# Kernel optimization log

Hardware: AMD Instinct MI355X
Metric: run time of the kernel (lower is better)

## Reference

```python
import jax, jax.numpy as jnp
import numpy as np
from jax.scipy.special import i0

# Module config (init_kwargs). sector_width only affects CUDA tiling, not math.
OSF = 2
KERNEL_WIDTH = 3
IMG_DIM = 320
B, M = 8, 200000


def setup_inputs() -> dict:
    key = jax.random.key(0)
    k1, k2, k3, k4 = jax.random.split(key, 4)
    x_re = jax.random.normal(k1, (B, IMG_DIM, IMG_DIM), jnp.float32)
    x_im = jax.random.normal(k2, (B, IMG_DIM, IMG_DIM), jnp.float32)
    # normalized k-space trajectory in [-0.5, 0.5) (gpuNUFFT convention)
    traj = jax.random.uniform(k3, (B, 2, M), jnp.float32, -0.5, 0.5)
    # density compensation weights, strictly positive
    dcf = jax.random.uniform(k4, (B, M), jnp.float32, 0.01, 1.0)
    return {"x_re": x_re, "x_im": x_im, "traj": traj, "dcf": dcf}


def _kb(d, W, beta):
    # Kaiser-Bessel gridding kernel, support |d| <= W/2 (d in oversampled grid units)
    t = jnp.clip(1.0 - (2.0 * d / W) ** 2, 0.0, None)
    return jnp.where(jnp.abs(d) <= W / 2.0, i0(beta * jnp.sqrt(t)), 0.0)


def _deapod_1d(N, G, W, beta):
    # Fourier transform of the KB kernel, sampled at image positions n/G
    xs = (jnp.arange(N, dtype=jnp.float32) - N // 2) / G
    arg = beta ** 2 - (jnp.pi * W * xs) ** 2
    s = jnp.sqrt(jnp.abs(arg))
    return jnp.where(arg > 0, jnp.sinh(s) / s, jnp.sinc(s / jnp.pi))


def _nufft_forward(x_re, x_im, traj, dcf):
    N, G, L = IMG_DIM, OSF * IMG_DIM, KERNEL_WIDTH
    W = float(KERNEL_WIDTH)
    # Beatty et al. optimal KB shape parameter
    beta = jnp.pi * np.sqrt((W / OSF) ** 2 * (OSF - 0.5) ** 2 - 0.8)

    # 1) deapodize image
    c = _deapod_1d(N, G, W, beta)  # [N]
    img = (x_re + 1j * x_im) / (c[:, None] * c[None, :])

    # 2) zero-pad to oversampled grid and FFT (centered)
    pad = (G - N) // 2
    img_p = jnp.pad(img, ((0, 0), (pad, pad), (pad, pad)))
    kgrid = jnp.fft.fftshift(
        jnp.fft.fft2(jnp.fft.ifftshift(img_p, axes=(1, 2)), axes=(1, 2)),
        axes=(1, 2)) / G  # [B,G,G]

    # 3) KB interpolation onto non-uniform samples
    coords = (traj + 0.5) * G                         # [B,2,M] in [0,G)
    offs = jnp.arange(L, dtype=jnp.float32)
    base = jnp.floor(coords - (L - 1) / 2.0)          # [B,2,M]
    idx = base[..., None] + offs                      # [B,2,M,L]
    d = coords[..., None] - idx                       # [B,2,M,L]
    w = _kb(d, W, beta)                               # [B,2,M,L]
    wx, wy = w[:, 0], w[:, 1]                         # x=cols, y=rows
    ix = idx[:, 0].astype(jnp.int32) % G              # [B,M,L]
    iy = idx[:, 1].astype(jnp.int32) % G
    flat = iy[:, :, :, None] * G + ix[:, :, None, :]  # [B,M,L,L]
    weights = wy[:, :, :, None] * wx[:, :, None, :]   # [B,M,L,L]
    vals = jax.vmap(lambda g, i: g[i])(kgrid.reshape(kgrid.shape[0], G * G), flat)
    k = jnp.sum(vals * weights.astype(vals.dtype), axis=(-1, -2))  # [B,M]

    # 4) density compensation (sqrt(dcf) weighting of forward samples)
    k = k * jnp.sqrt(dcf)
    return jnp.stack([k.real, k.imag], axis=-1)  # [B,M,2]


def reference(x_re, x_im, traj, dcf):
    return _nufft_forward(x_re, x_im, traj, dcf)
```

## Files before the change

kernel.cpp:

```cpp
#include <hip/hip_runtime.h>
#include <math.h>

#define GDIM 640
#define NDIM 320
#define NB 8
#define NM 200000
#define KROWS 643
#define KSTRIDE 644
#define PI_F 3.14159265358979323846f

__device__ __forceinline__ float bessel_i0f(float x) {
    if (x < 3.75f) {
        float t = x * (1.0f / 3.75f);
        t *= t;
        return 1.0f + t * (3.5156229f + t * (3.0899424f + t * (1.2067492f +
                     t * (0.2659732f + t * (0.0360768f + t * 0.0045813f)))));
    }
    float t = 3.75f / x;
    float p = 0.39894228f + t * (0.01328592f + t * (0.00225319f + t * (-0.00157565f +
              t * (0.00916281f + t * (-0.02057706f + t * (0.02635537f +
              t * (-0.01647633f + t * 0.00392377f)))))));
    return p * __expf(x) * rsqrtf(x);
}

__device__ __forceinline__ float deapod_c(int i, float beta2) {
    float xs = (float)(i - NDIM / 2) * (1.0f / (float)GDIM);
    float p = PI_F * 3.0f * xs;
    float arg = beta2 - p * p;
    float s = sqrtf(fabsf(arg));
    if (arg > 0.0f) return sinhf(s) / s;
    return (s < 1e-12f) ? 1.0f : sinf(s) / s;
}

__device__ __forceinline__ float kbw(float d, float beta) {
    if (fabsf(d) > 1.5f) return 0.0f;
    float u = d * (2.0f / 3.0f);
    float t = 1.0f - u * u;
    t = fmaxf(t, 0.0f);
    return bessel_i0f(beta * sqrtf(t));
}

__device__ __forceinline__ void build_tw(float2* tw, int tid) {
    for (int i = tid; i < 640; i += 320) {
        float sw, cw;
        __sincosf(-2.0f * PI_F * (float)i * (1.0f / 640.0f), &sw, &cw);
        tw[i] = make_float2(cw, sw);
    }
}

__device__ __forceinline__ void fft640_core(float2* lds, float2* lds2,
                                            const float2* tw, int tid) {
    if (tid < 128) {
        const int bb = tid;
        float2 xa[5];
#pragma unroll
        for (int a = 0; a < 5; ++a) xa[a] = lds[a * 128 + bb];
        const float c5[5] = {1.0f, 0.30901699f, -0.80901699f, -0.80901699f, 0.30901699f};
        const float s5[5] = {0.0f, -0.95105652f, -0.58778525f, 0.58778525f, 0.95105652f};
#pragma unroll
        for (int k1 = 0; k1 < 5; ++k1) {
            float2 acc = xa[0];
#pragma unroll
            for (int a = 1; a < 5; ++a) {
                int j = (a * k1) % 5;
                acc.x += xa[a].x * c5[j] - xa[a].y * s5[j];
                acc.y += xa[a].x * s5[j] + xa[a].y * c5[j];
            }
            float2 w = tw[bb * k1];
            float2 r;
            r.x = acc.x * w.x - acc.y * w.y;
            r.y = acc.x * w.y + acc.y * w.x;
            lds2[k1 * 128 + bb] = r;
        }
    }
    __syncthreads();

    const int f = tid >> 6;
    const int j = tid & 63;
    float2* arr = lds2 + f * 128;
#pragma unroll
    for (int h = 64; h >= 1; h >>= 1) {
        int g = j / h;
        int jj = j - g * h;
        int p = g * 2 * h + jj;
        float2 u = arr[p];
        float2 v = arr[p + h];
        float2 s = make_float2(u.x + v.x, u.y + v.y);
        float2 d = make_float2(u.x - v.x, u.y - v.y);
        float2 w = tw[jj * (320 / h)];
        arr[p] = s;
        arr[p + h] = make_float2(d.x * w.x - d.y * w.y, d.x * w.y + d.y * w.x);
        __syncthreads();
    }

#pragma unroll
    for (int half = 0; half < 2; ++half) {
        int k2 = j + 64 * half;
        int src = f * 128 + (int)(__brev((unsigned)k2) >> 25);
        int k = f + 5 * k2;
        int ks = (k >= 320) ? (k - 320) : (k + 320);
        lds[ks] = lds2[src];
    }
}

__global__ __launch_bounds__(320) void pass_a(const float* __restrict__ x_re,
                                              const float* __restrict__ x_im,
                                              float2* __restrict__ buf1c,
                                              float beta2) {
    __shared__ float2 lds[640];
    __shared__ float2 lds2[640];
    __shared__ float2 tw[640];
    const int b = blockIdx.y;
    const int r = blockIdx.x;
    const int tid = threadIdx.x;

    build_tw(tw, tid);

    const int ry = (r < 160) ? (r + 160) : (r - 160);
    const float cy = deapod_c(ry, beta2);
    const float scale = 1.0f / (cy * (float)GDIM);

    for (int i = tid; i < GDIM; i += 320) {
        int xx = (i >= 320) ? (i - 320) : (i + 320);
        float2 v = make_float2(0.0f, 0.0f);
        if (xx >= 160 && xx < 480) {
            int rx = xx - 160;
            float cx = deapod_c(rx, beta2);
            float sc = scale / cx;
            size_t off = ((size_t)b * NDIM + ry) * NDIM + rx;
            v.x = x_re[off] * sc;
            v.y = x_im[off] * sc;
        }
        lds[i] = v;
    }
    __syncthreads();

    fft640_core(lds, lds2, tw, tid);
    __syncthreads();

    float2* dst = buf1c + ((size_t)b * NDIM + r) * GDIM;
    for (int i = tid; i < GDIM; i += 320) dst[i] = lds[i];
}

__global__ __launch_bounds__(320) void pass_b(const float2* __restrict__ buf1c,
                                              float2* __restrict__ kbuf) {
    __shared__ float2 colsT[4][648];
    __shared__ float2 lds2[640];
    __shared__ float2 tw[640];
    const int b = blockIdx.y;
    const int kxs0 = blockIdx.x * 4;
    const int tid = threadIdx.x;

    build_tw(tw, tid);

    for (int base = 0; base < NDIM; base += 80) {
        int r = base + (tid >> 2);
        int c = tid & 3;
        float2 v = buf1c[((size_t)b * NDIM + r) * GDIM + kxs0 + c];
        int y = (r < 160) ? r : (r + 320);
        colsT[c][y] = v;
    }
    for (int i = tid; i < 1280; i += 320) {
        colsT[i & 3][160 + (i >> 2)] = make_float2(0.0f, 0.0f);
    }
    __syncthreads();

    float2* kbb = kbuf + (size_t)b * KROWS * KSTRIDE;

#pragma unroll
    for (int c = 0; c < 4; ++c) {
        fft640_core(&colsT[c][0], lds2, tw, tid);
        __syncthreads();

        const int kxs = kxs0 + c;
        int prs[2];
        int nduprow = 1;
        prs[0] = kxs + 1;
        if (kxs == 639) { prs[1] = 0;   nduprow = 2; }
        if (kxs == 0)   { prs[1] = 641; nduprow = 2; }
        if (kxs == 1)   { prs[1] = 642; nduprow = 2; }
        for (int rr = 0; rr < nduprow; ++rr) {
            float2* dst = kbb + (size_t)prs[rr] * KSTRIDE;
            for (int i = tid; i < GDIM; i += 320) dst[1 + i] = colsT[c][i];
            if (tid == 0) {
                dst[0]   = colsT[c][639];
                dst[641] = colsT[c][0];
                dst[642] = colsT[c][1];
            }
        }
        __syncthreads();
    }
}

#define GBLK_PER_B ((NM + 255) / 256)
__global__ __launch_bounds__(256) void gather_kernel(const float* __restrict__ traj,
                                                     const float* __restrict__ dcf,
                                                     const float2* __restrict__ kbuf,
                                                     float2* __restrict__ out,
                                                     float beta) {
    const int bid = blockIdx.x;
    const int b = bid & 7;
    const int m = (bid >> 3) * 256 + threadIdx.x;
    if (m >= NM) return;

    const float tx = traj[((size_t)b * 2 + 0) * NM + m];
    const float ty = traj[((size_t)b * 2 + 1) * NM + m];
    const float cx = (tx + 0.5f) * (float)GDIM;
    const float cy = (ty + 0.5f) * (float)GDIM;
    const int bxi = (int)floorf(cx - 1.0f);
    const int byi = (int)floorf(cy - 1.0f);
    const float fx = cx - (float)bxi;
    const float fy = cy - (float)byi;

    const float2* __restrict__ kb = kbuf + (size_t)b * KROWS * KSTRIDE;
    const int pc0 = byi + 1;
    const int odd = pc0 & 1;

    float4 A[3], Bv[3];
#pragma unroll
    for (int lx = 0; lx < 3; ++lx) {
        size_t e = ((size_t)(bxi + 1 + lx) * KSTRIDE + (size_t)pc0) & ~(size_t)1;
        const float4* p = (const float4*)(kb + e);
        A[lx] = p[0];
        Bv[lx] = p[1];
    }

    float wx[3], wy[3];
#pragma unroll
    for (int l = 0; l < 3; ++l) {
        wx[l] = kbw(fx - (float)l, beta);
        wy[l] = kbw(fy - (float)l, beta);
    }

    float accx = 0.0f, accy = 0.0f;
#pragma unroll
    for (int lx = 0; lx < 3; ++lx) {
        float t0x = odd ? A[lx].z : A[lx].x;
        float t0y = odd ? A[lx].w : A[lx].y;
        float t1x = odd ? Bv[lx].x : A[lx].z;
        float t1y = odd ? Bv[lx].y : A[lx].w;
        float t2x = odd ? Bv[lx].z : Bv[lx].x;
        float t2y = odd ? Bv[lx].w : Bv[lx].y;
        const float w0 = wx[lx] * wy[0];
        const float w1 = wx[lx] * wy[1];
        const float w2 = wx[lx] * wy[2];
        accx += t0x * w0 + t1x * w1 + t2x * w2;
        accy += t0y * w0 + t1y * w1 + t2y * w2;
    }
    const float s = sqrtf(dcf[(size_t)b * NM + m]);
    out[(size_t)b * NM + m] = make_float2(accx * s, accy * s);
}

extern "C" void kernel_launch(void* const* d_in, const int* in_sizes, int n_in,
                              void* d_out, int out_size, void* d_ws, size_t ws_size,
                              hipStream_t stream) {
    const float* x_re = (const float*)d_in[0];
    const float* x_im = (const float*)d_in[1];
    const float* traj = (const float*)d_in[2];
    const float* dcf  = (const float*)d_in[3];

    float2* buf1c = (float2*)d_ws;
    float2* kbuf  = buf1c + (size_t)NB * NDIM * GDIM;

    const double beta_d = M_PI * sqrt((1.5 * 1.5) * (1.5 * 1.5) - 0.8);
    const float beta = (float)beta_d;
    const float beta2 = (float)(beta_d * beta_d);

    dim3 gridA(NDIM, NB);
    pass_a<<<gridA, 320, 0, stream>>>(x_re, x_im, buf1c, beta2);

    dim3 gridB(GDIM / 4, NB);
    pass_b<<<gridB, 320, 0, stream>>>(buf1c, kbuf);

    gather_kernel<<<GBLK_PER_B * NB, 256, 0, stream>>>(traj, dcf, kbuf,
                                                       (float2*)d_out, beta);
}
```

Before: 82.12 us.

## Replace LDS radix-2 FFT stages with wavefront shuffle butterflies

```diff
diff --git a/kernel.cpp b/kernel.cpp
--- a/kernel.cpp
+++ b/kernel.cpp
@@ -40,67 +40,66 @@
     return bessel_i0f(beta * sqrtf(t));
 }
 
-__device__ __forceinline__ void build_tw(float2* tw, int tid) {
-    for (int i = tid; i < 640; i += 320) {
-        float sw, cw;
-        __sincosf(-2.0f * PI_F * (float)i * (1.0f / 640.0f), &sw, &cw);
-        tw[i] = make_float2(cw, sw);
-    }
-}
-
-__device__ __forceinline__ void fft640_core(float2* lds, float2* lds2,
-                                            const float2* tw, int tid) {
-    if (tid < 128) {
-        const int bb = tid;
-        float2 xa[5];
-#pragma unroll
-        for (int a = 0; a < 5; ++a) xa[a] = lds[a * 128 + bb];
-        const float c5[5] = {1.0f, 0.30901699f, -0.80901699f, -0.80901699f, 0.30901699f};
-        const float s5[5] = {0.0f, -0.95105652f, -0.58778525f, 0.58778525f, 0.95105652f};
-#pragma unroll
-        for (int k1 = 0; k1 < 5; ++k1) {
-            float2 acc = xa[0];
-#pragma unroll
-            for (int a = 1; a < 5; ++a) {
-                int j = (a * k1) % 5;
-                acc.x += xa[a].x * c5[j] - xa[a].y * s5[j];
-                acc.y += xa[a].x * s5[j] + xa[a].y * c5[j];
-            }
-            float2 w = tw[bb * k1];
-            float2 r;
-            r.x = acc.x * w.x - acc.y * w.y;
-            r.y = acc.x * w.y + acc.y * w.x;
-            lds2[k1 * 128 + bb] = r;
+__device__ __forceinline__ float2 cmul(float2 a, float2 b) {
+    return make_float2(a.x * b.x - a.y * b.y, a.x * b.y + a.y * b.x);
+}
+
+__device__ __forceinline__ void fft640_wave(float2* lds, int tid) {
+    const int f = tid >> 6;
+    const int L = tid & 63;
+    float sw, cw;
+
+    __sincosf(-2.0f * PI_F * (float)f * 0.2f, &sw, &cw);
+    const float2 w5 = make_float2(cw, sw);
+    float2 A = make_float2(0.0f, 0.0f), B = make_float2(0.0f, 0.0f);
+    float2 wa = make_float2(1.0f, 0.0f);
+#pragma unroll
+    for (int a = 0; a < 5; ++a) {
+        float2 xa = lds[a * 128 + L];
+        float2 xb = lds[a * 128 + L + 64];
+        A.x += xa.x * wa.x - xa.y * wa.y;  A.y += xa.x * wa.y + xa.y * wa.x;
+        B.x += xb.x * wa.x - xb.y * wa.y;  B.y += xb.x * wa.y + xb.y * wa.x;
+        wa = cmul(wa, w5);
+    }
+    __sincosf(-2.0f * PI_F * (float)(L * f) * (1.0f / 640.0f), &sw, &cw);
+    A = cmul(A, make_float2(cw, sw));
+    __sincosf(-2.0f * PI_F * (float)((L + 64) * f) * (1.0f / 640.0f), &sw, &cw);
+    B = cmul(B, make_float2(cw, sw));
+
+    {
+        float2 s = make_float2(A.x + B.x, A.y + B.y);
+        float2 d = make_float2(A.x - B.x, A.y - B.y);
+        __sincosf(-PI_F * (float)L * (1.0f / 64.0f), &sw, &cw);
+        B = cmul(d, make_float2(cw, sw));
+        A = s;
+    }
+#pragma unroll
+    for (int h = 32; h >= 1; h >>= 1) {
+        const int jj = L & (h - 1);
+        __sincosf(-PI_F * (float)jj * (1.0f / (float)h), &sw, &cw);
+        const float2 w = make_float2(cw, sw);
+        float2 Ao, Bo;
+        Ao.x = __shfl_xor(A.x, h, 64); Ao.y = __shfl_xor(A.y, h, 64);
+        Bo.x = __shfl_xor(B.x, h, 64); Bo.y = __shfl_xor(B.y, h, 64);
+        if ((L & h) == 0) {
+            A = make_float2(A.x + Ao.x, A.y + Ao.y);
+            B = make_float2(B.x + Bo.x, B.y + Bo.y);
+        } else {
+            A = cmul(make_float2(Ao.x - A.x, Ao.y - A.y), w);
+            B = cmul(make_float2(Bo.x - B.x, Bo.y - B.y), w);
         }
     }
-    __syncthreads();
-
-    const int f = tid >> 6;
-    const int j = tid & 63;
-    float2* arr = lds2 + f * 128;
-#pragma unroll
-    for (int h = 64; h >= 1; h >>= 1) {
-        int g = j / h;
-        int jj = j - g * h;
-        int p = g * 2 * h + jj;
-        float2 u = arr[p];
-        float2 v = arr[p + h];
-        float2 s = make_float2(u.x + v.x, u.y + v.y);
-        float2 d = make_float2(u.x - v.x, u.y - v.y);
-        float2 w = tw[jj * (320 / h)];
-        arr[p] = s;
-        arr[p + h] = make_float2(d.x * w.x - d.y * w.y, d.x * w.y + d.y * w.x);
-        __syncthreads();
-    }
-
-#pragma unroll
-    for (int half = 0; half < 2; ++half) {
-        int k2 = j + 64 * half;
-        int src = f * 128 + (int)(__brev((unsigned)k2) >> 25);
-        int k = f + 5 * k2;
-        int ks = (k >= 320) ? (k - 320) : (k + 320);
-        lds[ks] = lds2[src];
-    }
+
+    __syncthreads();
+
+    const int e = (int)(__brev((unsigned)L) >> 26);
+    const int ka = f + 10 * e;
+    const int kb = ka + 5;
+    const int ksa = (ka >= 320) ? (ka - 320) : (ka + 320);
+    const int ksb = (kb >= 320) ? (kb - 320) : (kb + 320);
+    lds[ksa] = A;
+    lds[ksb] = B;
+    __syncthreads();
 }
 
 __global__ __launch_bounds__(320) void pass_a(const float* __restrict__ x_re,
@@ -108,13 +107,9 @@
                                               float2* __restrict__ buf1c,
                                               float beta2) {
     __shared__ float2 lds[640];
-    __shared__ float2 lds2[640];
-    __shared__ float2 tw[640];
     const int b = blockIdx.y;
     const int r = blockIdx.x;
     const int tid = threadIdx.x;
-
-    build_tw(tw, tid);
 
     const int ry = (r < 160) ? (r + 160) : (r - 160);
     const float cy = deapod_c(ry, beta2);
@@ -135,8 +130,7 @@
     }
     __syncthreads();
 
-    fft640_core(lds, lds2, tw, tid);
-    __syncthreads();
+    fft640_wave(lds, tid);
 
     float2* dst = buf1c + ((size_t)b * NDIM + r) * GDIM;
     for (int i = tid; i < GDIM; i += 320) dst[i] = lds[i];
@@ -145,13 +139,9 @@
 __global__ __launch_bounds__(320) void pass_b(const float2* __restrict__ buf1c,
                                               float2* __restrict__ kbuf) {
     __shared__ float2 colsT[4][648];
-    __shared__ float2 lds2[640];
-    __shared__ float2 tw[640];
     const int b = blockIdx.y;
     const int kxs0 = blockIdx.x * 4;
     const int tid = threadIdx.x;
-
-    build_tw(tw, tid);
 
     for (int base = 0; base < NDIM; base += 80) {
         int r = base + (tid >> 2);
@@ -165,13 +155,14 @@
     }
     __syncthreads();
 
+#pragma unroll
+    for (int c = 0; c < 4; ++c) {
+        fft640_wave(&colsT[c][0], tid);
+    }
+
     float2* kbb = kbuf + (size_t)b * KROWS * KSTRIDE;
-
 #pragma unroll
     for (int c = 0; c < 4; ++c) {
-        fft640_core(&colsT[c][0], lds2, tw, tid);
-        __syncthreads();
-
         const int kxs = kxs0 + c;
         int prs[2];
         int nduprow = 1;
@@ -188,7 +179,6 @@
                 dst[642] = colsT[c][1];
             }
         }
-        __syncthreads();
     }
 }
 
```

Result: no change. 83.72 us (+2.0%).
